# Optimization experiments

Measured on AMD Instinct MI355X. Metric: run time of the kernel, lower is better.

The kernel has to match this reference:

```python
import jax, jax.numpy as jnp
import numpy as np

B, I, H, T = 1024, 256, 256, 64  # batch, input_size, SS/FS hidden, window


def setup_inputs() -> dict:
    key = jax.random.key(0)
    ks = jax.random.split(key, 12)
    s = 0.05
    return {
        "FS_output": jax.random.normal(ks[0], (B, T - 1, I), jnp.float32),
        "y_history": jax.random.normal(ks[1], (B, T - 1), jnp.float32),
        # linear_hidden: Linear(2H -> T)
        "W_h": jax.random.normal(ks[2], (2 * H, T), jnp.float32) * s,
        "b_h": jax.random.normal(ks[3], (T,), jnp.float32) * s,
        # linear_FS: Linear(T -> T)
        "W_fs": jax.random.normal(ks[4], (T, T), jnp.float32) * s,
        "b_fs": jax.random.normal(ks[5], (T,), jnp.float32) * s,
        # attn_layer: Linear(T -> 1)
        "W_attn": jax.random.normal(ks[6], (T, 1), jnp.float32) * s,
        "b_attn": jax.random.normal(ks[7], (1,), jnp.float32) * s,
        # LSTM cell params (torch gate order i,f,g,o)
        "W_ih": jax.random.normal(ks[8], (4 * H, I), jnp.float32) * s,
        "W_hh": jax.random.normal(ks[9], (4 * H, H), jnp.float32) * s,
        "b_ih": jax.random.normal(ks[10], (4 * H,), jnp.float32) * s,
        "b_hh": jax.random.normal(ks[11], (4 * H,), jnp.float32) * s,
    }


def reference(FS_output, y_history, W_h, b_h, W_fs, b_fs, W_attn, b_attn, W_ih, W_hh, b_ih, b_hh):
    Bv, Tm1, Iv = FS_output.shape
    Hv = W_hh.shape[1]
    # x_hat_part = cat(FS_output^T (B,I,T-1), y_t (B,I,1)); linear_FS is linear, so split:
    # time-invariant part computed once, y_t contribution added per step.
    fs_perm = jnp.swapaxes(FS_output, 1, 2)                 # (B, I, T-1)
    pre_fs = jnp.einsum('bit,tu->biu', fs_perm, W_fs[:-1]) + b_fs  # (B, I, T)
    w_fs_last = W_fs[-1]                                    # (T,)

    def step(carry, xs):
        h, c = carry                       # (B, H) each
        fs_t, y_t = xs                     # (B, I), (B,)
        hc = jnp.concatenate([h, c], axis=-1)              # (B, 2H)
        score_h = hc @ W_h + b_h                           # (B, T), same for every input row
        e = jnp.tanh(score_h[:, None, :] + pre_fs + y_t[:, None, None] * w_fs_last)  # (B, I, T)
        attn = (e @ W_attn)[..., 0] + b_attn[0]            # (B, I)
        a = jax.nn.softmax(attn, axis=-1)                  # (B, I)
        w_in = a * fs_t                                    # (B, I)
        gates = w_in @ W_ih.T + h @ W_hh.T + b_ih + b_hh   # (B, 4H)
        i_g, f_g, g_g, o_g = jnp.split(gates, 4, axis=-1)
        c_new = jax.nn.sigmoid(f_g) * c + jax.nn.sigmoid(i_g) * jnp.tanh(g_g)
        h_new = jax.nn.sigmoid(o_g) * jnp.tanh(c_new)
        return (h_new, c_new), (w_in, h_new)

    h0 = jnp.zeros((Bv, Hv), FS_output.dtype)
    xs = (jnp.swapaxes(FS_output, 0, 1), y_history.T)      # time-major
    _, (iw, ie) = jax.lax.scan(step, (h0, h0), xs)
    input_weighted = jnp.swapaxes(iw, 0, 1)                # (B, T-1, I)
    input_encoded = jnp.swapaxes(ie, 0, 1)                 # (B, T-1, H)
    return input_weighted, input_encoded
```

## Files before the change

### kernel.cpp

```cpp
#include <hip/hip_runtime.h>
#include <hip/hip_bf16.h>

#define NB 1024
#define NI 256
#define NH 256
#define NT 64
#define TM1 63

typedef short bf16x8 __attribute__((ext_vector_type(8)));
typedef float f32x4 __attribute__((ext_vector_type(4)));

__device__ __forceinline__ float bf2f(__hip_bfloat16 x){ return __bfloat162float(x); }
__device__ __forceinline__ float bf16s_to_f(short s){
    unsigned u = ((unsigned)(unsigned short)s) << 16;
    return __builtin_bit_cast(float, u);
}
__device__ __forceinline__ unsigned short f_to_bf16s(float f){
    __hip_bfloat16 h = __float2bfloat16(f);
    return *(unsigned short*)&h;
}
__device__ __forceinline__ unsigned pack_bf16(float lo, float hi){
    return (unsigned)f_to_bf16s(lo) | ((unsigned)f_to_bf16s(hi) << 16);
}

__device__ __forceinline__ float fast_exp2(float x){ return __builtin_amdgcn_exp2f(x); }
__device__ __forceinline__ float fast_rcp(float x){ return __builtin_amdgcn_rcpf(x); }
__device__ __forceinline__ float fast_tanh(float x){
    float e = fast_exp2(x * 2.8853900817779268f);
    return 1.f - 2.f * fast_rcp(e + 1.f);
}
__device__ __forceinline__ float fast_sigmoid(float x){
    return fast_rcp(1.f + fast_exp2(-1.4426950408889634f * x));
}

__global__ __launch_bounds__(256) void prep_w2(
    const float* __restrict__ Wih, const float* __restrict__ Whh,
    const float* __restrict__ bih, const float* __restrict__ bhh,
    const float* __restrict__ Wh,
    __hip_bfloat16* __restrict__ W2, float* __restrict__ bias,
    __hip_bfloat16* __restrict__ Wh3)
{
    int tid = threadIdx.x;
    if (blockIdx.x < 1024){
        int n = blockIdx.x;
        W2[(long)n*512 + tid]       = __float2bfloat16(Wih[(long)n*256 + tid]);
        W2[(long)n*512 + 256 + tid] = __float2bfloat16(Whh[(long)n*256 + tid]);
        if (tid == 0) bias[n] = bih[n] + bhh[n];
    } else {
        int idx = (blockIdx.x - 1024) * 256 + tid;
        int k  = idx & 31;
        int u  = (idx >> 5) & 63;
        int jt = idx >> 11;
        float v = (k < 16) ? Wh[(jt*16 + k)*NT + u]
                           : Wh[(256 + jt*16 + (k - 16))*NT + u];
        Wh3[idx] = __float2bfloat16(v);
    }
}

__global__ __launch_bounds__(256) void prefs_kernel(
    const float* __restrict__ FS,
    const float* __restrict__ Wfs,
    const float* __restrict__ bfs,
    __hip_bfloat16* __restrict__ prefsT)
{
    __shared__ float wfs_s[TM1][NT];
    int b = blockIdx.x, tid = threadIdx.x;
    for (int idx = tid; idx < TM1*NT; idx += 256)
        wfs_s[idx >> 6][idx & 63] = Wfs[idx];
    __syncthreads();

    const float* fsp = FS + (long)b*TM1*NI + tid;

    f32x4 acc[16];
    #pragma unroll
    for (int g = 0; g < 16; ++g) acc[g] = *(const f32x4*)(bfs + g*4);

    #pragma unroll 4
    for (int t = 0; t < TM1; ++t){
        float fs = fsp[(long)t*NI];
        #pragma unroll
        for (int g = 0; g < 16; ++g){
            f32x4 w4 = *(const f32x4*)&wfs_s[t][g*4];
            acc[g] += fs * w4;
        }
    }

    uint4* dst = (uint4*)(prefsT + ((long)b*NI + tid)*NT);
    #pragma unroll
    for (int g = 0; g < 16; g += 2){
        uint4 v;
        v.x = pack_bf16(acc[g][0],   acc[g][1]);
        v.y = pack_bf16(acc[g][2],   acc[g][3]);
        v.z = pack_bf16(acc[g+1][0], acc[g+1][1]);
        v.w = pack_bf16(acc[g+1][2], acc[g+1][3]);
        dst[g >> 1] = v;
    }
}

__global__ __launch_bounds__(256) void attn_kernel(
    int t,
    const float* __restrict__ FS,
    const float* __restrict__ yhist,
    const float* __restrict__ bh,
    const float* __restrict__ Wfs,
    const float* __restrict__ Wattn,
    const float* __restrict__ battn,
    const __hip_bfloat16* __restrict__ prefsT,
    const float* __restrict__ s2part,
    __hip_bfloat16* __restrict__ Xcur,
    float* __restrict__ out_iw)
{
    __shared__ float s2_s[NT];
    __shared__ float wattn_s[NT];
    __shared__ float s2red[4][NT];
    __shared__ float red[4];
    int b = blockIdx.x, tid = threadIdx.x;
    int wid = tid >> 6;

    const bf16x8* pfT = (const bf16x8*)(prefsT + ((long)b*NI + tid)*NT);
    bf16x8 pf[8];
    #pragma unroll
    for (int o = 0; o < 8; ++o) pf[o] = pfT[o];

    {
        int u = tid & 63, grp = wid;
        float acc4 = 0.f;
        #pragma unroll
        for (int q = 0; q < 4; ++q)
            acc4 += s2part[((long)(grp + 4*q)*NB + b)*NT + u];
        s2red[grp][u] = acc4;
    }
    __syncthreads();
    if (tid < NT){
        float y = yhist[b*TM1 + t];
        s2_s[tid] = s2red[0][tid] + s2red[1][tid] + s2red[2][tid] + s2red[3][tid]
                  + bh[tid] + y * Wfs[TM1*NT + tid];
        wattn_s[tid] = Wattn[tid];
    }
    __syncthreads();

    float acc = 0.f;
    #pragma unroll
    for (int o = 0; o < 8; ++o){
        #pragma unroll
        for (int j = 0; j < 8; ++j){
            float x = s2_s[o*8 + j] + bf16s_to_f(pf[o][j]);
            acc = fmaf(fast_tanh(x), wattn_s[o*8 + j], acc);
        }
    }
    float attn = acc + battn[0];

    float m = attn;
    #pragma unroll
    for (int o = 32; o > 0; o >>= 1) m = fmaxf(m, __shfl_xor(m, o, 64));
    if ((tid & 63) == 0) red[wid] = m;
    __syncthreads();
    m = fmaxf(fmaxf(red[0], red[1]), fmaxf(red[2], red[3]));
    __syncthreads();
    float p = fast_exp2((attn - m) * 1.4426950408889634f);
    float ssum = p;
    #pragma unroll
    for (int o = 32; o > 0; o >>= 1) ssum += __shfl_xor(ssum, o, 64);
    if ((tid & 63) == 0) red[wid] = ssum;
    __syncthreads();
    ssum = red[0] + red[1] + red[2] + red[3];
    float a = p * fast_rcp(ssum);

    float w = a * FS[((long)b*TM1 + t)*NI + tid];
    Xcur[b*512 + tid] = __float2bfloat16(w);
    out_iw[((long)b*TM1 + t)*NI + tid] = w;
}

__global__ __launch_bounds__(256) void gates_kernel(
    int t,
    const __hip_bfloat16* __restrict__ W2,
    const float* __restrict__ bias,
    const __hip_bfloat16* __restrict__ Wh3,
    const __hip_bfloat16* __restrict__ Xcur,
    float* __restrict__ c,
    __hip_bfloat16* __restrict__ Xnext,
    float* __restrict__ s2part,
    float* __restrict__ out_ie)
{
    __shared__ __hip_bfloat16 hc_lds[64][32];

    int tid  = threadIdx.x;
    int wave = tid >> 6, lane = tid & 63;
    int bx = blockIdx.x, by = blockIdx.y;
    int m0 = bx * 64 + wave * 16;
    int j0 = by * 16;
    int lm = lane & 15;
    int lk = (lane >> 4) * 8;

    f32x4 acc[4] = {};
    const __hip_bfloat16* xrow = Xcur + (long)(m0 + lm) * 512;

    for (int kc = 0; kc < 16; ++kc){
        int kb = kc * 32 + lk;
        bf16x8 afrag = *(const bf16x8*)(xrow + kb);
        #pragma unroll
        for (int q = 0; q < 4; ++q){
            int ncol = q * 256 + j0 + lm;
            bf16x8 bfrag = *(const bf16x8*)(W2 + (long)ncol * 512 + kb);
            acc[q] = __builtin_amdgcn_mfma_f32_16x16x32_bf16(afrag, bfrag, acc[q], 0, 0, 0);
        }
    }

    int j = j0 + lm;
    float bb[4];
    #pragma unroll
    for (int q = 0; q < 4; ++q) bb[q] = bias[q*256 + j];

    #pragma unroll
    for (int r = 0; r < 4; ++r){
        int mloc = wave*16 + (lane >> 4)*4 + r;
        int m = bx*64 + mloc;
        float ig = acc[0][r] + bb[0];
        float fg = acc[1][r] + bb[1];
        float gg = acc[2][r] + bb[2];
        float og = acc[3][r] + bb[3];
        float cold = c[m*NH + j];
        float cn = fast_sigmoid(fg) * cold + fast_sigmoid(ig) * fast_tanh(gg);
        float hn = fast_sigmoid(og) * fast_tanh(cn);
        c[m*NH + j] = cn;
        Xnext[(long)m*512 + 256 + j] = __float2bfloat16(hn);
        out_ie[((long)m*TM1 + t)*NH + j] = hn;
        hc_lds[mloc][lm]      = __float2bfloat16(hn);
        hc_lds[mloc][16 + lm] = __float2bfloat16(cn);
    }
    __syncthreads();

    bf16x8 af = *(const bf16x8*)&hc_lds[wave*16 + lm][lk];
    f32x4 sacc[4] = {};
    #pragma unroll
    for (int nt = 0; nt < 4; ++nt){
        bf16x8 bfrag = *(const bf16x8*)(Wh3 + ((long)by*64 + nt*16 + lm)*32 + lk);
        sacc[nt] = __builtin_amdgcn_mfma_f32_16x16x32_bf16(af, bfrag, sacc[nt], 0, 0, 0);
    }
    #pragma unroll
    for (int nt = 0; nt < 4; ++nt){
        int u = nt*16 + lm;
        #pragma unroll
        for (int r = 0; r < 4; ++r){
            int m = bx*64 + wave*16 + (lane >> 4)*4 + r;
            s2part[((long)by*NB + m)*NT + u] = sacc[nt][r];
        }
    }
}

extern "C" void kernel_launch(void* const* d_in, const int* in_sizes, int n_in,
                              void* d_out, int out_size, void* d_ws, size_t ws_size,
                              hipStream_t stream)
{
    const float* FS    = (const float*)d_in[0];
    const float* yh    = (const float*)d_in[1];
    const float* Wh    = (const float*)d_in[2];
    const float* bh    = (const float*)d_in[3];
    const float* Wfs   = (const float*)d_in[4];
    const float* bfs   = (const float*)d_in[5];
    const float* Wattn = (const float*)d_in[6];
    const float* battn = (const float*)d_in[7];
    const float* Wih   = (const float*)d_in[8];
    const float* Whh   = (const float*)d_in[9];
    const float* bih   = (const float*)d_in[10];
    const float* bhh   = (const float*)d_in[11];

    char* ws = (char*)d_ws;
    const size_t MB = 1048576;
    __hip_bfloat16* prefsT = (__hip_bfloat16*)ws;
    size_t off = (size_t)NB * NI * NT * sizeof(__hip_bfloat16);
    __hip_bfloat16* X0  = (__hip_bfloat16*)(ws + off);
    float* c            = (float*)(ws + off + 1*MB);
    float* s2part       = (float*)(ws + off + 2*MB);
    __hip_bfloat16* X1  = (__hip_bfloat16*)(ws + off + 6*MB);
    __hip_bfloat16* W2  = (__hip_bfloat16*)(ws + off + 7*MB);
    float* bias         = (float*)(ws + off + 8*MB);
    __hip_bfloat16* Wh3 = (__hip_bfloat16*)(ws + off + 8*MB + 4096);
    __hip_bfloat16* Xb[2] = {X0, X1};

    float* out_iw = (float*)d_out;
    float* out_ie = out_iw + (size_t)NB * TM1 * NI;

    hipMemsetAsync(ws + off, 0, 6*MB, stream);

    prep_w2<<<1152, 256, 0, stream>>>(Wih, Whh, bih, bhh, Wh, W2, bias, Wh3);
    prefs_kernel<<<NB, 256, 0, stream>>>(FS, Wfs, bfs, prefsT);

    for (int t = 0; t < TM1; ++t){
        __hip_bfloat16* Xcur  = Xb[t & 1];
        __hip_bfloat16* Xnext = Xb[(t + 1) & 1];
        attn_kernel<<<NB, 256, 0, stream>>>(t, FS, yh, bh, Wfs, Wattn, battn,
                                            prefsT, s2part, Xcur, out_iw);
        gates_kernel<<<dim3(16,16), 256, 0, stream>>>(t, W2, bias, Wh3,
                                                      Xcur, c, Xnext, s2part, out_ie);
    }
}
```

Before: 1.800 ms.

## Replace per-step kernel launches with persistent cooperative kernel and grid barriers

Merges the attention and gates kernels into one persistent cooperative kernel of 256 blocks × 1024 threads that loops over all 63 time steps. A custom atomic grid barrier separates the phases, replacing 126 kernel launches. The gates GEMM is redistributed so each wave computes one gate tile, with results staged through LDS. This removes launch overhead and inter-kernel gaps, at the cost of spin-wait barriers and fewer resident blocks during the attention phase.

Measured after the change: 6.909 ms. 284% more time.

```diff
diff --git a/kernel.cpp b/kernel.cpp
--- a/kernel.cpp
+++ b/kernel.cpp
@@ -7,10 +7,12 @@
 #define NT 64
 #define TM1 63
 
+#define GRID_BLOCKS 256
+#define BLOCK_THREADS 1024
+
 typedef short bf16x8 __attribute__((ext_vector_type(8)));
 typedef float f32x4 __attribute__((ext_vector_type(4)));
 
-__device__ __forceinline__ float bf2f(__hip_bfloat16 x){ return __bfloat162float(x); }
 __device__ __forceinline__ float bf16s_to_f(short s){
     unsigned u = ((unsigned)(unsigned short)s) << 16;
     return __builtin_bit_cast(float, u);
@@ -31,6 +33,32 @@
 }
 __device__ __forceinline__ float fast_sigmoid(float x){
     return fast_rcp(1.f + fast_exp2(-1.4426950408889634f * x));
+}
+
+__device__ __forceinline__ void gridbar(int* arrive, int* release_, int gen){
+    __syncthreads();
+    int tid = threadIdx.x;
+    if (tid == 0){
+        __threadfence();
+        __hip_atomic_store(&arrive[blockIdx.x], gen,
+                           __ATOMIC_RELEASE, __HIP_MEMORY_SCOPE_AGENT);
+    }
+    if (blockIdx.x == 0){
+        if (tid < GRID_BLOCKS){
+            while (__hip_atomic_load(&arrive[tid],
+                     __ATOMIC_ACQUIRE, __HIP_MEMORY_SCOPE_AGENT) < gen) {}
+        }
+        __syncthreads();
+        if (tid == 0)
+            __hip_atomic_store(release_, gen,
+                               __ATOMIC_RELEASE, __HIP_MEMORY_SCOPE_AGENT);
+    }
+    if (tid == 0){
+        while (__hip_atomic_load(release_,
+                 __ATOMIC_ACQUIRE, __HIP_MEMORY_SCOPE_AGENT) < gen) {}
+        __threadfence();
+    }
+    __syncthreads();
 }
 
 __global__ __launch_bounds__(256) void prep_w2(
@@ -97,8 +125,7 @@
     }
 }
 
-__global__ __launch_bounds__(256) void attn_kernel(
-    int t,
+__global__ __launch_bounds__(BLOCK_THREADS, 4) void persist_kernel(
     const float* __restrict__ FS,
     const float* __restrict__ yhist,
     const float* __restrict__ bh,
@@ -106,145 +133,163 @@
     const float* __restrict__ Wattn,
     const float* __restrict__ battn,
     const __hip_bfloat16* __restrict__ prefsT,
-    const float* __restrict__ s2part,
-    __hip_bfloat16* __restrict__ Xcur,
-    float* __restrict__ out_iw)
-{
-    __shared__ float s2_s[NT];
-    __shared__ float wattn_s[NT];
-    __shared__ float s2red[4][NT];
-    __shared__ float red[4];
-    int b = blockIdx.x, tid = threadIdx.x;
-    int wid = tid >> 6;
-
-    const bf16x8* pfT = (const bf16x8*)(prefsT + ((long)b*NI + tid)*NT);
-    bf16x8 pf[8];
-    #pragma unroll
-    for (int o = 0; o < 8; ++o) pf[o] = pfT[o];
-
-    {
-        int u = tid & 63, grp = wid;
-        float acc4 = 0.f;
-        #pragma unroll
-        for (int q = 0; q < 4; ++q)
-            acc4 += s2part[((long)(grp + 4*q)*NB + b)*NT + u];
-        s2red[grp][u] = acc4;
-    }
-    __syncthreads();
-    if (tid < NT){
-        float y = yhist[b*TM1 + t];
-        s2_s[tid] = s2red[0][tid] + s2red[1][tid] + s2red[2][tid] + s2red[3][tid]
-                  + bh[tid] + y * Wfs[TM1*NT + tid];
-        wattn_s[tid] = Wattn[tid];
-    }
-    __syncthreads();
-
-    float acc = 0.f;
-    #pragma unroll
-    for (int o = 0; o < 8; ++o){
-        #pragma unroll
-        for (int j = 0; j < 8; ++j){
-            float x = s2_s[o*8 + j] + bf16s_to_f(pf[o][j]);
-            acc = fmaf(fast_tanh(x), wattn_s[o*8 + j], acc);
-        }
-    }
-    float attn = acc + battn[0];
-
-    float m = attn;
-    #pragma unroll
-    for (int o = 32; o > 0; o >>= 1) m = fmaxf(m, __shfl_xor(m, o, 64));
-    if ((tid & 63) == 0) red[wid] = m;
-    __syncthreads();
-    m = fmaxf(fmaxf(red[0], red[1]), fmaxf(red[2], red[3]));
-    __syncthreads();
-    float p = fast_exp2((attn - m) * 1.4426950408889634f);
-    float ssum = p;
-    #pragma unroll
-    for (int o = 32; o > 0; o >>= 1) ssum += __shfl_xor(ssum, o, 64);
-    if ((tid & 63) == 0) red[wid] = ssum;
-    __syncthreads();
-    ssum = red[0] + red[1] + red[2] + red[3];
-    float a = p * fast_rcp(ssum);
-
-    float w = a * FS[((long)b*TM1 + t)*NI + tid];
-    Xcur[b*512 + tid] = __float2bfloat16(w);
-    out_iw[((long)b*TM1 + t)*NI + tid] = w;
-}
-
-__global__ __launch_bounds__(256) void gates_kernel(
-    int t,
     const __hip_bfloat16* __restrict__ W2,
     const float* __restrict__ bias,
     const __hip_bfloat16* __restrict__ Wh3,
-    const __hip_bfloat16* __restrict__ Xcur,
-    float* __restrict__ c,
-    __hip_bfloat16* __restrict__ Xnext,
+    __hip_bfloat16* __restrict__ X0,
+    __hip_bfloat16* __restrict__ X1,
+    float* __restrict__ cbuf,
     float* __restrict__ s2part,
+    int* arrive, int* release_,
+    float* __restrict__ out_iw,
     float* __restrict__ out_ie)
 {
-    __shared__ __hip_bfloat16 hc_lds[64][32];
-
-    int tid  = threadIdx.x;
-    int wave = tid >> 6, lane = tid & 63;
-    int bx = blockIdx.x, by = blockIdx.y;
-    int m0 = bx * 64 + wave * 16;
-    int j0 = by * 16;
-    int lm = lane & 15;
-    int lk = (lane >> 4) * 8;
-
-    f32x4 acc[4] = {};
-    const __hip_bfloat16* xrow = Xcur + (long)(m0 + lm) * 512;
-
-    for (int kc = 0; kc < 16; ++kc){
-        int kb = kc * 32 + lk;
-        bf16x8 afrag = *(const bf16x8*)(xrow + kb);
-        #pragma unroll
-        for (int q = 0; q < 4; ++q){
-            int ncol = q * 256 + j0 + lm;
-            bf16x8 bfrag = *(const bf16x8*)(W2 + (long)ncol * 512 + kb);
-            acc[q] = __builtin_amdgcn_mfma_f32_16x16x32_bf16(afrag, bfrag, acc[q], 0, 0, 0);
+    __shared__ float2 s2w[4][NT];
+    __shared__ float  s2red[4][4][NT];
+    __shared__ float  red_m[4][4], red_s[4][4];
+    __shared__ float  bh_s[NT], wfsl_s[NT], wattn_s[NT];
+    __shared__ float  battn_s;
+    __shared__ float  bias_s[4][16];
+    __shared__ float  gates_lds[4][64][17];
+    __shared__ __hip_bfloat16 hcmini[64][40];
+
+    int tid = threadIdx.x;
+    int blk = blockIdx.x;
+
+    int g     = tid >> 8;
+    int it    = tid & 255;
+    int b     = blk*4 + g;
+    int gw    = it >> 6;
+    int lane6 = it & 63;
+
+    int wv   = tid >> 6, lane = tid & 63;
+    int msub = wv & 3, q = wv >> 2;
+    int mt   = blk >> 4, jt = blk & 15;
+    int lm   = lane & 15, lk = (lane >> 4) * 8;
+    int mloc = tid >> 4, jl = tid & 15;
+
+    if (tid < NT){
+        bh_s[tid]    = bh[tid];
+        wfsl_s[tid]  = Wfs[TM1*NT + tid];
+        wattn_s[tid] = Wattn[tid];
+        bias_s[tid >> 4][tid & 15] = bias[(tid >> 4)*256 + jt*16 + (tid & 15)];
+    }
+    if (tid == 64) battn_s = battn[0];
+    __syncthreads();
+
+    int gen = 0;
+
+    for (int t = 0; t < TM1; ++t){
+        __hip_bfloat16* Xc = (t & 1) ? X1 : X0;
+        __hip_bfloat16* Xn = (t & 1) ? X0 : X1;
+
+        {
+            const bf16x8* pfT = (const bf16x8*)(prefsT + ((long)b*NI + it)*NT);
+            bf16x8 pf[8];
+            #pragma unroll
+            for (int o = 0; o < 8; ++o) pf[o] = pfT[o];
+
+            {
+                float acc4 = 0.f;
+                #pragma unroll
+                for (int qq = 0; qq < 4; ++qq)
+                    acc4 += s2part[((long)(gw + 4*qq)*NB + b)*NT + lane6];
+                s2red[g][gw][lane6] = acc4;
+            }
+            __syncthreads();
+            if (it < NT){
+                float y = yhist[b*TM1 + t];
+                float s2v = s2red[g][0][it] + s2red[g][1][it]
+                          + s2red[g][2][it] + s2red[g][3][it]
+                          + bh_s[it] + y * wfsl_s[it];
+                s2w[g][it] = make_float2(s2v, wattn_s[it]);
+            }
+            __syncthreads();
+
+            float acc = 0.f;
+            #pragma unroll
+            for (int o = 0; o < 8; ++o){
+                #pragma unroll
+                for (int j = 0; j < 8; ++j){
+                    float2 sw = s2w[g][o*8 + j];
+                    float x = sw.x + bf16s_to_f(pf[o][j]);
+                    acc = fmaf(fast_tanh(x), sw.y, acc);
+                }
+            }
+            float attn = acc + battn_s;
+
+            float mx = attn;
+            #pragma unroll
+            for (int o = 32; o > 0; o >>= 1) mx = fmaxf(mx, __shfl_xor(mx, o, 64));
+            if (lane6 == 0) red_m[g][gw] = mx;
+            __syncthreads();
+            mx = fmaxf(fmaxf(red_m[g][0], red_m[g][1]),
+                       fmaxf(red_m[g][2], red_m[g][3]));
+            float p = fast_exp2((attn - mx) * 1.4426950408889634f);
+            float ss = p;
+            #pragma unroll
+            for (int o = 32; o > 0; o >>= 1) ss += __shfl_xor(ss, o, 64);
+            if (lane6 == 0) red_s[g][gw] = ss;
+            __syncthreads();
+            ss = red_s[g][0] + red_s[g][1] + red_s[g][2] + red_s[g][3];
+            float a = p * fast_rcp(ss);
+
+            float w = a * FS[((long)b*TM1 + t)*NI + it];
+            Xc[b*512 + it] = __float2bfloat16(w);
+            out_iw[((long)b*TM1 + t)*NI + it] = w;
         }
-    }
-
-    int j = j0 + lm;
-    float bb[4];
-    #pragma unroll
-    for (int q = 0; q < 4; ++q) bb[q] = bias[q*256 + j];
-
-    #pragma unroll
-    for (int r = 0; r < 4; ++r){
-        int mloc = wave*16 + (lane >> 4)*4 + r;
-        int m = bx*64 + mloc;
-        float ig = acc[0][r] + bb[0];
-        float fg = acc[1][r] + bb[1];
-        float gg = acc[2][r] + bb[2];
-        float og = acc[3][r] + bb[3];
-        float cold = c[m*NH + j];
-        float cn = fast_sigmoid(fg) * cold + fast_sigmoid(ig) * fast_tanh(gg);
-        float hn = fast_sigmoid(og) * fast_tanh(cn);
-        c[m*NH + j] = cn;
-        Xnext[(long)m*512 + 256 + j] = __float2bfloat16(hn);
-        out_ie[((long)m*TM1 + t)*NH + j] = hn;
-        hc_lds[mloc][lm]      = __float2bfloat16(hn);
-        hc_lds[mloc][16 + lm] = __float2bfloat16(cn);
-    }
-    __syncthreads();
-
-    bf16x8 af = *(const bf16x8*)&hc_lds[wave*16 + lm][lk];
-    f32x4 sacc[4] = {};
-    #pragma unroll
-    for (int nt = 0; nt < 4; ++nt){
-        bf16x8 bfrag = *(const bf16x8*)(Wh3 + ((long)by*64 + nt*16 + lm)*32 + lk);
-        sacc[nt] = __builtin_amdgcn_mfma_f32_16x16x32_bf16(af, bfrag, sacc[nt], 0, 0, 0);
-    }
-    #pragma unroll
-    for (int nt = 0; nt < 4; ++nt){
-        int u = nt*16 + lm;
-        #pragma unroll
-        for (int r = 0; r < 4; ++r){
-            int m = bx*64 + wave*16 + (lane >> 4)*4 + r;
-            s2part[((long)by*NB + m)*NT + u] = sacc[nt][r];
+
+        gridbar(arrive, release_, ++gen);
+
+        {
+            int m0 = mt*64 + msub*16;
+            const __hip_bfloat16* xrow = Xc + (long)(m0 + lm) * 512;
+            const __hip_bfloat16* wrow = W2 + (long)(q*256 + jt*16 + lm) * 512;
+            f32x4 acc = {};
+            #pragma unroll
+            for (int kc = 0; kc < 16; ++kc){
+                bf16x8 afrag = *(const bf16x8*)(xrow + kc*32 + lk);
+                bf16x8 bfrag = *(const bf16x8*)(wrow + kc*32 + lk);
+                acc = __builtin_amdgcn_mfma_f32_16x16x32_bf16(afrag, bfrag, acc, 0, 0, 0);
+            }
+            {
+                int row0 = msub*16 + (lane >> 4)*4;
+                #pragma unroll
+                for (int r = 0; r < 4; ++r)
+                    gates_lds[q][row0 + r][lm] = acc[r];
+            }
+            __syncthreads();
+            {
+                int m = mt*64 + mloc, j = jt*16 + jl;
+                float ig = gates_lds[0][mloc][jl] + bias_s[0][jl];
+                float fg = gates_lds[1][mloc][jl] + bias_s[1][jl];
+                float gg = gates_lds[2][mloc][jl] + bias_s[2][jl];
+                float og = gates_lds[3][mloc][jl] + bias_s[3][jl];
+                float cold = cbuf[m*NH + j];
+                float cn = fast_sigmoid(fg) * cold + fast_sigmoid(ig) * fast_tanh(gg);
+                float hn = fast_sigmoid(og) * fast_tanh(cn);
+                cbuf[m*NH + j] = cn;
+                Xn[(long)m*512 + 256 + j] = __float2bfloat16(hn);
+                out_ie[((long)m*TM1 + t)*NH + j] = hn;
+                hcmini[mloc][jl]      = __float2bfloat16(hn);
+                hcmini[mloc][16 + jl] = __float2bfloat16(cn);
+            }
+            __syncthreads();
+            {
+                bf16x8 af = *(const bf16x8*)&hcmini[msub*16 + lm][lk];
+                bf16x8 bfrag = *(const bf16x8*)(Wh3 + ((long)jt*64 + q*16 + lm)*32 + lk);
+                f32x4 sacc = {};
+                sacc = __builtin_amdgcn_mfma_f32_16x16x32_bf16(af, bfrag, sacc, 0, 0, 0);
+                int u = q*16 + lm;
+                #pragma unroll
+                for (int r = 0; r < 4; ++r){
+                    int m = mt*64 + msub*16 + (lane >> 4)*4 + r;
+                    s2part[((long)jt*NB + m)*NT + u] = sacc[r];
+                }
+            }
         }
+
+        if (t < TM1 - 1) gridbar(arrive, release_, ++gen);
     }
 }
 
@@ -270,28 +315,30 @@
     __hip_bfloat16* prefsT = (__hip_bfloat16*)ws;
     size_t off = (size_t)NB * NI * NT * sizeof(__hip_bfloat16);
     __hip_bfloat16* X0  = (__hip_bfloat16*)(ws + off);
-    float* c            = (float*)(ws + off + 1*MB);
+    float* cbuf         = (float*)(ws + off + 1*MB);
     float* s2part       = (float*)(ws + off + 2*MB);
-    __hip_bfloat16* X1  = (__hip_bfloat16*)(ws + off + 6*MB);
-    __hip_bfloat16* W2  = (__hip_bfloat16*)(ws + off + 7*MB);
-    float* bias         = (float*)(ws + off + 8*MB);
-    __hip_bfloat16* Wh3 = (__hip_bfloat16*)(ws + off + 8*MB + 4096);
-    __hip_bfloat16* Xb[2] = {X0, X1};
+    int*   arrive       = (int*)(ws + off + 6*MB);
+    int*   release_     = (int*)(ws + off + 6*MB + 2048);
+    __hip_bfloat16* X1  = (__hip_bfloat16*)(ws + off + 7*MB);
+    __hip_bfloat16* W2  = (__hip_bfloat16*)(ws + off + 8*MB);
+    float* bias         = (float*)(ws + off + 9*MB);
+    __hip_bfloat16* Wh3 = (__hip_bfloat16*)(ws + off + 9*MB + 4096);
 
     float* out_iw = (float*)d_out;
     float* out_ie = out_iw + (size_t)NB * TM1 * NI;
 
-    hipMemsetAsync(ws + off, 0, 6*MB, stream);
+    hipMemsetAsync(ws + off, 0, 6*MB + 4096, stream);
 
     prep_w2<<<1152, 256, 0, stream>>>(Wih, Whh, bih, bhh, Wh, W2, bias, Wh3);
     prefs_kernel<<<NB, 256, 0, stream>>>(FS, Wfs, bfs, prefsT);
 
-    for (int t = 0; t < TM1; ++t){
-        __hip_bfloat16* Xcur  = Xb[t & 1];
-        __hip_bfloat16* Xnext = Xb[(t + 1) & 1];
-        attn_kernel<<<NB, 256, 0, stream>>>(t, FS, yh, bh, Wfs, Wattn, battn,
-                                            prefsT, s2part, Xcur, out_iw);
-        gates_kernel<<<dim3(16,16), 256, 0, stream>>>(t, W2, bias, Wh3,
-                                                      Xcur, c, Xnext, s2part, out_ie);
-    }
-}
+    void* args[] = {
+        (void*)&FS, (void*)&yh, (void*)&bh, (void*)&Wfs, (void*)&Wattn,
+        (void*)&battn, (void*)&prefsT, (void*)&W2, (void*)&bias, (void*)&Wh3,
+        (void*)&X0, (void*)&X1, (void*)&cbuf, (void*)&s2part,
+        (void*)&arrive, (void*)&release_, (void*)&out_iw, (void*)&out_ie
+    };
+    hipLaunchCooperativeKernel(reinterpret_cast<void*>(persist_kernel),
+                               dim3(GRID_BLOCKS), dim3(BLOCK_THREADS),
+                               args, 0, stream);
+}
```

## Fuse all timesteps into one persistent recurrent kernel over batch groups

Applied to the files above, without the earlier changes.

Replaces 126 per-timestep attn/gates kernel launches with a single persistent kernel where each block owns 4 batch rows and loops over all 63 timesteps, keeping h, c and the attention score in LDS. This removes launch overhead and global round-trips for s2part, X buffers and the c state, and drops the workspace memset. In exchange each block re-reads the full W2 (1 MB bf16) and WhT from global/L2 every timestep, and uses only 256 blocks with 4-row MFMA tiles that waste most of the 16-row M dimension.

After: 5.309 ms. +194.9%, slower.

```diff
diff --git a/kernel.cpp b/kernel.cpp
--- a/kernel.cpp
+++ b/kernel.cpp
@@ -10,7 +10,6 @@
 typedef short bf16x8 __attribute__((ext_vector_type(8)));
 typedef float f32x4 __attribute__((ext_vector_type(4)));
 
-__device__ __forceinline__ float bf2f(__hip_bfloat16 x){ return __bfloat162float(x); }
 __device__ __forceinline__ float bf16s_to_f(short s){
     unsigned u = ((unsigned)(unsigned short)s) << 16;
     return __builtin_bit_cast(float, u);
@@ -38,7 +37,7 @@
     const float* __restrict__ bih, const float* __restrict__ bhh,
     const float* __restrict__ Wh,
     __hip_bfloat16* __restrict__ W2, float* __restrict__ bias,
-    __hip_bfloat16* __restrict__ Wh3)
+    __hip_bfloat16* __restrict__ WhT)
 {
     int tid = threadIdx.x;
     if (blockIdx.x < 1024){
@@ -48,12 +47,9 @@
         if (tid == 0) bias[n] = bih[n] + bhh[n];
     } else {
         int idx = (blockIdx.x - 1024) * 256 + tid;
-        int k  = idx & 31;
-        int u  = (idx >> 5) & 63;
-        int jt = idx >> 11;
-        float v = (k < 16) ? Wh[(jt*16 + k)*NT + u]
-                           : Wh[(256 + jt*16 + (k - 16))*NT + u];
-        Wh3[idx] = __float2bfloat16(v);
+        int u = idx >> 9;
+        int k = idx & 511;
+        WhT[idx] = __float2bfloat16(Wh[k*NT + u]);
     }
 }
 
@@ -97,8 +93,7 @@
     }
 }
 
-__global__ __launch_bounds__(256) void attn_kernel(
-    int t,
+__global__ __launch_bounds__(256, 1) void recurrent_kernel(
     const float* __restrict__ FS,
     const float* __restrict__ yhist,
     const float* __restrict__ bh,
@@ -106,145 +101,173 @@
     const float* __restrict__ Wattn,
     const float* __restrict__ battn,
     const __hip_bfloat16* __restrict__ prefsT,
-    const float* __restrict__ s2part,
-    __hip_bfloat16* __restrict__ Xcur,
-    float* __restrict__ out_iw)
-{
-    __shared__ float s2_s[NT];
-    __shared__ float wattn_s[NT];
-    __shared__ float s2red[4][NT];
-    __shared__ float red[4];
-    int b = blockIdx.x, tid = threadIdx.x;
-    int wid = tid >> 6;
-
-    const bf16x8* pfT = (const bf16x8*)(prefsT + ((long)b*NI + tid)*NT);
-    bf16x8 pf[8];
-    #pragma unroll
-    for (int o = 0; o < 8; ++o) pf[o] = pfT[o];
-
-    {
-        int u = tid & 63, grp = wid;
-        float acc4 = 0.f;
-        #pragma unroll
-        for (int q = 0; q < 4; ++q)
-            acc4 += s2part[((long)(grp + 4*q)*NB + b)*NT + u];
-        s2red[grp][u] = acc4;
-    }
-    __syncthreads();
-    if (tid < NT){
-        float y = yhist[b*TM1 + t];
-        s2_s[tid] = s2red[0][tid] + s2red[1][tid] + s2red[2][tid] + s2red[3][tid]
-                  + bh[tid] + y * Wfs[TM1*NT + tid];
-        wattn_s[tid] = Wattn[tid];
-    }
-    __syncthreads();
-
-    float acc = 0.f;
-    #pragma unroll
-    for (int o = 0; o < 8; ++o){
-        #pragma unroll
-        for (int j = 0; j < 8; ++j){
-            float x = s2_s[o*8 + j] + bf16s_to_f(pf[o][j]);
-            acc = fmaf(fast_tanh(x), wattn_s[o*8 + j], acc);
-        }
-    }
-    float attn = acc + battn[0];
-
-    float m = attn;
-    #pragma unroll
-    for (int o = 32; o > 0; o >>= 1) m = fmaxf(m, __shfl_xor(m, o, 64));
-    if ((tid & 63) == 0) red[wid] = m;
-    __syncthreads();
-    m = fmaxf(fmaxf(red[0], red[1]), fmaxf(red[2], red[3]));
-    __syncthreads();
-    float p = fast_exp2((attn - m) * 1.4426950408889634f);
-    float ssum = p;
-    #pragma unroll
-    for (int o = 32; o > 0; o >>= 1) ssum += __shfl_xor(ssum, o, 64);
-    if ((tid & 63) == 0) red[wid] = ssum;
-    __syncthreads();
-    ssum = red[0] + red[1] + red[2] + red[3];
-    float a = p * fast_rcp(ssum);
-
-    float w = a * FS[((long)b*TM1 + t)*NI + tid];
-    Xcur[b*512 + tid] = __float2bfloat16(w);
-    out_iw[((long)b*TM1 + t)*NI + tid] = w;
-}
-
-__global__ __launch_bounds__(256) void gates_kernel(
-    int t,
     const __hip_bfloat16* __restrict__ W2,
     const float* __restrict__ bias,
-    const __hip_bfloat16* __restrict__ Wh3,
-    const __hip_bfloat16* __restrict__ Xcur,
-    float* __restrict__ c,
-    __hip_bfloat16* __restrict__ Xnext,
-    float* __restrict__ s2part,
+    const __hip_bfloat16* __restrict__ WhT,
+    float* __restrict__ out_iw,
     float* __restrict__ out_ie)
 {
-    __shared__ __hip_bfloat16 hc_lds[64][32];
+    __shared__ __align__(16) __hip_bfloat16 hcx[4][520];
+    __shared__ __align__(16) __hip_bfloat16 hc2[4][520];
+    __shared__ __align__(16) float c_s[4][264];
+    __shared__ __align__(16) float gates_s[4][1032];
+    __shared__ __align__(16) float s2_s[4][72];
+    __shared__ __align__(16) float bias_s[1024];
+    __shared__ __align__(16) float bh_s[NT], wfsl_s[NT], wattn_s[NT];
+    __shared__ float yv[4];
+    __shared__ float redm[4][4], reds[4][4];
+    __shared__ float battn_s;
 
     int tid  = threadIdx.x;
+    int b0   = blockIdx.x * 4;
     int wave = tid >> 6, lane = tid & 63;
-    int bx = blockIdx.x, by = blockIdx.y;
-    int m0 = bx * 64 + wave * 16;
-    int j0 = by * 16;
-    int lm = lane & 15;
-    int lk = (lane >> 4) * 8;
-
-    f32x4 acc[4] = {};
-    const __hip_bfloat16* xrow = Xcur + (long)(m0 + lm) * 512;
-
-    for (int kc = 0; kc < 16; ++kc){
-        int kb = kc * 32 + lk;
-        bf16x8 afrag = *(const bf16x8*)(xrow + kb);
-        #pragma unroll
-        for (int q = 0; q < 4; ++q){
-            int ncol = q * 256 + j0 + lm;
-            bf16x8 bfrag = *(const bf16x8*)(W2 + (long)ncol * 512 + kb);
-            acc[q] = __builtin_amdgcn_mfma_f32_16x16x32_bf16(afrag, bfrag, acc[q], 0, 0, 0);
-        }
-    }
-
-    int j = j0 + lm;
-    float bb[4];
-    #pragma unroll
-    for (int q = 0; q < 4; ++q) bb[q] = bias[q*256 + j];
-
-    #pragma unroll
-    for (int r = 0; r < 4; ++r){
-        int mloc = wave*16 + (lane >> 4)*4 + r;
-        int m = bx*64 + mloc;
-        float ig = acc[0][r] + bb[0];
-        float fg = acc[1][r] + bb[1];
-        float gg = acc[2][r] + bb[2];
-        float og = acc[3][r] + bb[3];
-        float cold = c[m*NH + j];
-        float cn = fast_sigmoid(fg) * cold + fast_sigmoid(ig) * fast_tanh(gg);
-        float hn = fast_sigmoid(og) * fast_tanh(cn);
-        c[m*NH + j] = cn;
-        Xnext[(long)m*512 + 256 + j] = __float2bfloat16(hn);
-        out_ie[((long)m*TM1 + t)*NH + j] = hn;
-        hc_lds[mloc][lm]      = __float2bfloat16(hn);
-        hc_lds[mloc][16 + lm] = __float2bfloat16(cn);
+    int lm   = lane & 15, lk = (lane >> 4) * 8;
+    int brow = lm & 3;
+
+    for (int idx = tid; idx < 1024; idx += 256) bias_s[idx] = bias[idx];
+    if (tid < NT){
+        bh_s[tid]    = bh[tid];
+        wfsl_s[tid]  = Wfs[TM1*NT + tid];
+        wattn_s[tid] = Wattn[tid];
+    }
+    if (tid == 64) battn_s = battn[0];
+    {
+        int b = tid >> 6, j = tid & 63;
+        #pragma unroll
+        for (int p = 0; p < 4; ++p){
+            int jj = j + p*64;
+            hcx[b][256+jj] = __float2bfloat16(0.f);
+            hc2[b][jj]     = __float2bfloat16(0.f);
+            hc2[b][256+jj] = __float2bfloat16(0.f);
+            c_s[b][jj]     = 0.f;
+        }
     }
     __syncthreads();
 
-    bf16x8 af = *(const bf16x8*)&hc_lds[wave*16 + lm][lk];
-    f32x4 sacc[4] = {};
-    #pragma unroll
-    for (int nt = 0; nt < 4; ++nt){
-        bf16x8 bfrag = *(const bf16x8*)(Wh3 + ((long)by*64 + nt*16 + lm)*32 + lk);
-        sacc[nt] = __builtin_amdgcn_mfma_f32_16x16x32_bf16(af, bfrag, sacc[nt], 0, 0, 0);
-    }
-    #pragma unroll
-    for (int nt = 0; nt < 4; ++nt){
-        int u = nt*16 + lm;
-        #pragma unroll
-        for (int r = 0; r < 4; ++r){
-            int m = bx*64 + wave*16 + (lane >> 4)*4 + r;
-            s2part[((long)by*NB + m)*NT + u] = sacc[nt][r];
-        }
+    for (int t = 0; t < TM1; ++t){
+        if (tid < 4) yv[tid] = yhist[(b0 + tid)*TM1 + t];
+
+        {
+            int u0 = wave * 16;
+            const __hip_bfloat16* wrow = WhT + (long)(u0 + lm)*512 + lk;
+            f32x4 sacc = {};
+            #pragma unroll
+            for (int kc = 0; kc < 16; ++kc){
+                bf16x8 af = *(const bf16x8*)&hc2[brow][kc*32 + lk];
+                bf16x8 bf = *(const bf16x8*)(wrow + kc*32);
+                sacc = __builtin_amdgcn_mfma_f32_16x16x32_bf16(af, bf, sacc, 0, 0, 0);
+            }
+            if (lane < 16){
+                #pragma unroll
+                for (int r = 0; r < 4; ++r) s2_s[r][u0 + lane] = sacc[r];
+            }
+        }
+        __syncthreads();
+        {
+            int bb = wave, u = lane;
+            s2_s[bb][u] += bh_s[u] + yv[bb] * wfsl_s[u];
+        }
+        __syncthreads();
+
+        float attnv[4];
+        #pragma unroll
+        for (int bb = 0; bb < 4; ++bb){
+            const bf16x8* pfT = (const bf16x8*)(prefsT + ((long)(b0+bb)*NI + tid)*NT);
+            bf16x8 pf[8];
+            #pragma unroll
+            for (int o = 0; o < 8; ++o) pf[o] = pfT[o];
+            float acc0 = 0.f, acc1 = 0.f;
+            #pragma unroll
+            for (int o = 0; o < 8; ++o){
+                f32x4 sa = *(const f32x4*)&s2_s[bb][o*8];
+                f32x4 sb = *(const f32x4*)&s2_s[bb][o*8 + 4];
+                f32x4 wa = *(const f32x4*)&wattn_s[o*8];
+                f32x4 wb = *(const f32x4*)&wattn_s[o*8 + 4];
+                #pragma unroll
+                for (int j = 0; j < 4; ++j){
+                    acc0 = fmaf(fast_tanh(sa[j] + bf16s_to_f(pf[o][j])),   wa[j], acc0);
+                    acc1 = fmaf(fast_tanh(sb[j] + bf16s_to_f(pf[o][j+4])), wb[j], acc1);
+                }
+            }
+            attnv[bb] = acc0 + acc1 + battn_s;
+        }
+
+        #pragma unroll
+        for (int bb = 0; bb < 4; ++bb){
+            float m = attnv[bb];
+            #pragma unroll
+            for (int o = 32; o > 0; o >>= 1) m = fmaxf(m, __shfl_xor(m, o, 64));
+            if (lane == 0) redm[bb][wave] = m;
+        }
+        __syncthreads();
+        float fsv[4], pv[4];
+        #pragma unroll
+        for (int bb = 0; bb < 4; ++bb)
+            fsv[bb] = FS[((long)(b0+bb)*TM1 + t)*NI + tid];
+        #pragma unroll
+        for (int bb = 0; bb < 4; ++bb){
+            float m = fmaxf(fmaxf(redm[bb][0], redm[bb][1]),
+                            fmaxf(redm[bb][2], redm[bb][3]));
+            float p = fast_exp2((attnv[bb] - m) * 1.4426950408889634f);
+            pv[bb] = p;
+            float ss = p;
+            #pragma unroll
+            for (int o = 32; o > 0; o >>= 1) ss += __shfl_xor(ss, o, 64);
+            if (lane == 0) reds[bb][wave] = ss;
+        }
+        __syncthreads();
+        #pragma unroll
+        for (int bb = 0; bb < 4; ++bb){
+            float ss = reds[bb][0] + reds[bb][1] + reds[bb][2] + reds[bb][3];
+            float w = pv[bb] * fast_rcp(ss) * fsv[bb];
+            hcx[bb][tid] = __float2bfloat16(w);
+            out_iw[((long)(b0+bb)*TM1 + t)*NI + tid] = w;
+        }
+        __syncthreads();
+
+        {
+            bf16x8 Af[16];
+            #pragma unroll
+            for (int kc = 0; kc < 16; ++kc)
+                Af[kc] = *(const bf16x8*)&hcx[brow][kc*32 + lk];
+
+            #pragma unroll 2
+            for (int d = 0; d < 16; ++d){
+                int n0 = wave*256 + d*16;
+                const __hip_bfloat16* wp = W2 + (long)(n0 + lm)*512 + lk;
+                f32x4 acc = {};
+                #pragma unroll
+                for (int kc = 0; kc < 16; ++kc){
+                    bf16x8 bfrag = *(const bf16x8*)(wp + kc*32);
+                    acc = __builtin_amdgcn_mfma_f32_16x16x32_bf16(Af[kc], bfrag, acc, 0, 0, 0);
+                }
+                if (lane < 16){
+                    #pragma unroll
+                    for (int r = 0; r < 4; ++r) gates_s[r][n0 + lane] = acc[r];
+                }
+            }
+        }
+        __syncthreads();
+        {
+            int bb = wave;
+            #pragma unroll
+            for (int p = 0; p < 4; ++p){
+                int j = lane + p*64;
+                float ig = gates_s[bb][j]       + bias_s[j];
+                float fg = gates_s[bb][256 + j] + bias_s[256 + j];
+                float gg = gates_s[bb][512 + j] + bias_s[512 + j];
+                float og = gates_s[bb][768 + j] + bias_s[768 + j];
+                float cold = c_s[bb][j];
+                float cn = fast_sigmoid(fg)*cold + fast_sigmoid(ig)*fast_tanh(gg);
+                float hn = fast_sigmoid(og)*fast_tanh(cn);
+                c_s[bb][j]     = cn;
+                hcx[bb][256+j] = __float2bfloat16(hn);
+                hc2[bb][j]     = __float2bfloat16(hn);
+                hc2[bb][256+j] = __float2bfloat16(cn);
+                out_ie[((long)(b0+bb)*TM1 + t)*NH + j] = hn;
+            }
+        }
+        __syncthreads();
     }
 }
 
@@ -269,29 +292,16 @@
     const size_t MB = 1048576;
     __hip_bfloat16* prefsT = (__hip_bfloat16*)ws;
     size_t off = (size_t)NB * NI * NT * sizeof(__hip_bfloat16);
-    __hip_bfloat16* X0  = (__hip_bfloat16*)(ws + off);
-    float* c            = (float*)(ws + off + 1*MB);
-    float* s2part       = (float*)(ws + off + 2*MB);
-    __hip_bfloat16* X1  = (__hip_bfloat16*)(ws + off + 6*MB);
-    __hip_bfloat16* W2  = (__hip_bfloat16*)(ws + off + 7*MB);
-    float* bias         = (float*)(ws + off + 8*MB);
-    __hip_bfloat16* Wh3 = (__hip_bfloat16*)(ws + off + 8*MB + 4096);
-    __hip_bfloat16* Xb[2] = {X0, X1};
+    __hip_bfloat16* W2  = (__hip_bfloat16*)(ws + off);
+    float* bias         = (float*)(ws + off + 1*MB);
+    __hip_bfloat16* WhT = (__hip_bfloat16*)(ws + off + 1*MB + 4096);
 
     float* out_iw = (float*)d_out;
     float* out_ie = out_iw + (size_t)NB * TM1 * NI;
 
-    hipMemsetAsync(ws + off, 0, 6*MB, stream);
-
-    prep_w2<<<1152, 256, 0, stream>>>(Wih, Whh, bih, bhh, Wh, W2, bias, Wh3);
+    prep_w2<<<1152, 256, 0, stream>>>(Wih, Whh, bih, bhh, Wh, W2, bias, WhT);
     prefs_kernel<<<NB, 256, 0, stream>>>(FS, Wfs, bfs, prefsT);
-
-    for (int t = 0; t < TM1; ++t){
-        __hip_bfloat16* Xcur  = Xb[t & 1];
-        __hip_bfloat16* Xnext = Xb[(t + 1) & 1];
-        attn_kernel<<<NB, 256, 0, stream>>>(t, FS, yh, bh, Wfs, Wattn, battn,
-                                            prefsT, s2part, Xcur, out_iw);
-        gates_kernel<<<dim3(16,16), 256, 0, stream>>>(t, W2, bias, Wh3,
-                                                      Xcur, c, Xnext, s2part, out_ie);
-    }
-}
+    recurrent_kernel<<<256, 256, 0, stream>>>(FS, yh, bh, Wfs, Wattn, battn,
+                                              prefsT, W2, bias, WhT,
+                                              out_iw, out_ie);
+}
```
